# Kernel tuning notes

Measured on AMD Instinct MI355X. Metric: run time of the kernel, lower is better.

Reference implementation:

```python
import jax, jax.numpy as jnp
import numpy as np

B, S, H = 32, 512, 1024
N_CAND = 256
NUM_LABELS = 34


def setup_inputs() -> dict:
    key = jax.random.key(0)
    k1, k2, k3, k4 = jax.random.split(key, 4)
    hidden = jax.random.normal(k1, (B, S, H), dtype=jnp.float32)
    W = jax.random.normal(k2, (2 * H, NUM_LABELS), dtype=jnp.float32) * 0.02
    b = jnp.zeros((NUM_LABELS,), dtype=jnp.float32)
    cand_batch = jax.random.randint(k3, (N_CAND,), 0, B, dtype=jnp.int32)
    # cut positions in [1, S-1] so both left and right segments are non-empty
    cand_cut = jax.random.randint(k4, (N_CAND,), 1, S, dtype=jnp.int32)
    return {"hidden": hidden, "W": W, "b": b,
            "cand_batch": cand_batch, "cand_cut": cand_cut}


def reference(hidden, W, b, cand_batch, cand_cut):
    # hidden: [B, S, H]; cand_batch/cand_cut: [N]
    S_ = hidden.shape[1]
    x = hidden[cand_batch]                      # [N, S, H] per-candidate sequence
    pos = jnp.arange(S_)                        # [S]
    left = (pos[None, :, None] < cand_cut[:, None, None])  # [N, S, 1]
    neg = jnp.finfo(hidden.dtype).min
    pooledL = jnp.max(jnp.where(left, x, neg), axis=1)      # [N, H] max over tokens < cut
    pooledR = jnp.max(jnp.where(left, neg, x), axis=1)      # [N, H] max over tokens >= cut
    pooled = jnp.concatenate([pooledL, pooledR], axis=-1)   # [N, 2H]
    logits = pooled @ W + b                                  # [N, num_labels]
    return logits
```

## Files before the change

kernel.cpp:

```cpp
#include <hip/hip_runtime.h>
#include <cfloat>


constexpr int S_LEN  = 512;
constexpr int HDIM   = 1024;
constexpr int NLAB   = 34;
constexpr int CHUNK  = 16;
constexpr int NCHUNK = S_LEN / CHUNK;

__device__ __forceinline__ void fmax4(float4& a, const float4 v) {
    a.x = fmaxf(a.x, v.x); a.y = fmaxf(a.y, v.y);
    a.z = fmaxf(a.z, v.z); a.w = fmaxf(a.w, v.w);
}

__global__ __launch_bounds__(256) void chunkmax_kernel(
    const float* __restrict__ hidden, float* __restrict__ ws0)
{
    const int blk = blockIdx.x;
    const int b   = blk / NCHUNK;
    const int c   = blk % NCHUNK;
    const int t   = threadIdx.x;

    const float* base = hidden + ((size_t)b * S_LEN + (size_t)c * CHUNK) * HDIM + 4 * t;
    float4 m = make_float4(-FLT_MAX, -FLT_MAX, -FLT_MAX, -FLT_MAX);
    #pragma unroll
    for (int s = 0; s < CHUNK; ++s)
        fmax4(m, *reinterpret_cast<const float4*>(base + (size_t)s * HDIM));

    *reinterpret_cast<float4*>(ws0 + ((size_t)b * NCHUNK + c) * HDIM + 4 * t) = m;
}

__global__ __launch_bounds__(1024) void pool_gemm2(
    const float* __restrict__ hidden,
    const float* __restrict__ ws0,
    const float* __restrict__ W,
    const float* __restrict__ bias,
    const int*   __restrict__ cand_batch,
    const int*   __restrict__ cand_cut,
    float*       __restrict__ out)
{
    __shared__ float partL[4][HDIM];
    __shared__ float partR[4][HDIM];
    __shared__ float pooled[2 * HDIM];
    __shared__ float gpart[16][NLAB];

    const int n   = blockIdx.x;
    const int t   = threadIdx.x;
    const int g   = t >> 8;
    const int tt  = t & 255;
    const int col = 4 * tt;
    const int b   = cand_batch[n];
    const int cut = cand_cut[n];
    const int fcL = cut >> 4;
    const int fcR = (cut + CHUNK - 1) >> 4;

    const float* hbase = hidden + (size_t)b * S_LEN * HDIM + col;
    const float* wbase = ws0 + (size_t)b * NCHUNK * HDIM + col;

    float4 mL = make_float4(-FLT_MAX, -FLT_MAX, -FLT_MAX, -FLT_MAX);
    float4 mR = mL;

    #pragma unroll 2
    for (int c = g; c < fcL; c += 4)
        fmax4(mL, *reinterpret_cast<const float4*>(wbase + (size_t)c * HDIM));
    const int c0 = fcR + ((g - fcR) & 3);
    #pragma unroll 2
    for (int c = c0; c < NCHUNK; c += 4)
        fmax4(mR, *reinterpret_cast<const float4*>(wbase + (size_t)c * HDIM));

    #pragma unroll 2
    for (int s = fcL * CHUNK + g; s < cut; s += 4)
        fmax4(mL, *reinterpret_cast<const float4*>(hbase + (size_t)s * HDIM));
    #pragma unroll 2
    for (int s = cut + g; s < fcR * CHUNK; s += 4)
        fmax4(mR, *reinterpret_cast<const float4*>(hbase + (size_t)s * HDIM));

    *reinterpret_cast<float4*>(&partL[g][col]) = mL;
    *reinterpret_cast<float4*>(&partR[g][col]) = mR;
    __syncthreads();

    {
        const int j = t;
        pooled[j] = fmaxf(fmaxf(partL[0][j], partL[1][j]),
                          fmaxf(partL[2][j], partL[3][j]));
        pooled[HDIM + j] = fmaxf(fmaxf(partR[0][j], partR[1][j]),
                                 fmaxf(partR[2][j], partR[3][j]));
    }
    __syncthreads();

    const int w    = t >> 6;
    const int lane = t & 63;
    if (lane < NLAB) {
        const float* p = pooled + 128 * w;
        const float* Wp = W + (size_t)(128 * w) * NLAB + lane;
        float acc = 0.0f;
        #pragma unroll 8
        for (int k = 0; k < 128; ++k)
            acc = fmaf(p[k], Wp[(size_t)k * NLAB], acc);
        gpart[w][lane] = acc;
    }
    __syncthreads();

    if (t < NLAB) {
        float s = bias[t];
        #pragma unroll
        for (int w2 = 0; w2 < 16; ++w2) s += gpart[w2][t];
        out[(size_t)n * NLAB + t] = s;
    }
}

__global__ __launch_bounds__(256) void dmbert_pool_gemm(
    const float* __restrict__ hidden,
    const float* __restrict__ W,
    const float* __restrict__ bias,
    const int*   __restrict__ cand_batch,
    const int*   __restrict__ cand_cut,
    float*       __restrict__ out)
{
    __shared__ float pooled[2 * HDIM];
    __shared__ float partial[4][NLAB];

    const int n   = blockIdx.x;
    const int t   = threadIdx.x;
    const int bi  = cand_batch[n];
    const int cut = cand_cut[n];

    const float* base = hidden + (size_t)bi * S_LEN * HDIM + 4 * t;
    float4 mL = make_float4(-FLT_MAX, -FLT_MAX, -FLT_MAX, -FLT_MAX);
    float4 mR = mL;

    #pragma unroll 4
    for (int s = 0; s < cut; ++s)
        fmax4(mL, *reinterpret_cast<const float4*>(base + (size_t)s * HDIM));
    #pragma unroll 4
    for (int s = cut; s < S_LEN; ++s)
        fmax4(mR, *reinterpret_cast<const float4*>(base + (size_t)s * HDIM));

    *reinterpret_cast<float4*>(&pooled[4 * t])        = mL;
    *reinterpret_cast<float4*>(&pooled[HDIM + 4 * t]) = mR;
    __syncthreads();

    const int w    = t >> 6;
    const int lane = t & 63;
    if (lane < NLAB) {
        const int k0 = w * (2 * HDIM / 4);
        float acc = 0.0f;
        #pragma unroll 8
        for (int k = k0; k < k0 + (2 * HDIM / 4); ++k)
            acc = fmaf(pooled[k], W[(size_t)k * NLAB + lane], acc);
        partial[w][lane] = acc;
    }
    __syncthreads();

    if (t < NLAB) {
        out[(size_t)n * NLAB + t] =
            partial[0][t] + partial[1][t] + partial[2][t] + partial[3][t] + bias[t];
    }
}

extern "C" void kernel_launch(void* const* d_in, const int* in_sizes, int n_in,
                              void* d_out, int out_size, void* d_ws, size_t ws_size,
                              hipStream_t stream) {
    const float* hidden = (const float*)d_in[0];
    const float* W      = (const float*)d_in[1];
    const float* bias   = (const float*)d_in[2];
    const int*   cb     = (const int*)d_in[3];
    const int*   cc     = (const int*)d_in[4];
    float*       outp   = (float*)d_out;

    const int ncand = in_sizes[3];
    const int B     = in_sizes[0] / (S_LEN * HDIM);
    const size_t ws_needed = (size_t)B * NCHUNK * HDIM * sizeof(float);

    if (ws_size >= ws_needed) {
        float* cm = (float*)d_ws;
        chunkmax_kernel<<<B * NCHUNK, 256, 0, stream>>>(hidden, cm);
        pool_gemm2<<<ncand, 1024, 0, stream>>>(hidden, cm, W, bias, cb, cc, outp);
    } else {
        dmbert_pool_gemm<<<ncand, 256, 0, stream>>>(hidden, W, bias, cb, cc, outp);
    }
}
```

Measured before the change: 107.5 us.

## Precompute prefix/suffix chunk maxima so each candidate reads one row per side

Adds a kernel that builds running prefix and suffix maxima over the per-chunk maxima for each batch. The pooling kernel then takes the full-chunk part of each side from a single precomputed row and scans only the one partial chunk at the cut. This removes the per-candidate loops over up to 32 chunk rows. In exchange it adds a third launch, a serial 32-step scan in a small grid (128 blocks of 128 threads), and extra workspace traffic.

```diff
diff --git a/kernel.cpp b/kernel.cpp
--- a/kernel.cpp
+++ b/kernel.cpp
@@ -7,6 +7,7 @@
 constexpr int NLAB   = 34;
 constexpr int CHUNK  = 16;
 constexpr int NCHUNK = S_LEN / CHUNK;
+constexpr int PSDIM  = NCHUNK + 1;
 
 __device__ __forceinline__ void fmax4(float4& a, const float4 v) {
     a.x = fmaxf(a.x, v.x); a.y = fmaxf(a.y, v.y);
@@ -14,7 +15,7 @@
 }
 
 __global__ __launch_bounds__(256) void chunkmax_kernel(
-    const float* __restrict__ hidden, float* __restrict__ ws0)
+    const float* __restrict__ hidden, float* __restrict__ cm)
 {
     const int blk = blockIdx.x;
     const int b   = blk / NCHUNK;
@@ -27,12 +28,47 @@
     for (int s = 0; s < CHUNK; ++s)
         fmax4(m, *reinterpret_cast<const float4*>(base + (size_t)s * HDIM));
 
-    *reinterpret_cast<float4*>(ws0 + ((size_t)b * NCHUNK + c) * HDIM + 4 * t) = m;
-}
-
-__global__ __launch_bounds__(1024) void pool_gemm2(
+    *reinterpret_cast<float4*>(cm + ((size_t)b * NCHUNK + c) * HDIM + 4 * t) = m;
+}
+
+__global__ __launch_bounds__(128) void prefsuf_kernel(
+    const float* __restrict__ cm,
+    float* __restrict__ pref,
+    float* __restrict__ suff)
+{
+    const int b    = blockIdx.x;
+    const int q    = blockIdx.y;
+    const int tx   = threadIdx.x;
+    const int dir  = tx >> 6;
+    const int lane = tx & 63;
+    const int col  = q * 256 + 4 * lane;
+
+    const float* cmb = cm + (size_t)b * NCHUNK * HDIM + col;
+    float4 run = make_float4(-FLT_MAX, -FLT_MAX, -FLT_MAX, -FLT_MAX);
+
+    if (dir == 0) {
+        float* pb = pref + (size_t)b * PSDIM * HDIM + col;
+        *reinterpret_cast<float4*>(pb) = run;
+        #pragma unroll 8
+        for (int c = 0; c < NCHUNK; ++c) {
+            fmax4(run, *reinterpret_cast<const float4*>(cmb + (size_t)c * HDIM));
+            *reinterpret_cast<float4*>(pb + (size_t)(c + 1) * HDIM) = run;
+        }
+    } else {
+        float* sb = suff + (size_t)b * PSDIM * HDIM + col;
+        *reinterpret_cast<float4*>(sb + (size_t)NCHUNK * HDIM) = run;
+        #pragma unroll 8
+        for (int c = NCHUNK - 1; c >= 0; --c) {
+            fmax4(run, *reinterpret_cast<const float4*>(cmb + (size_t)c * HDIM));
+            *reinterpret_cast<float4*>(sb + (size_t)c * HDIM) = run;
+        }
+    }
+}
+
+__global__ __launch_bounds__(1024) void pool_gemm3(
     const float* __restrict__ hidden,
-    const float* __restrict__ ws0,
+    const float* __restrict__ pref,
+    const float* __restrict__ suff,
     const float* __restrict__ W,
     const float* __restrict__ bias,
     const int*   __restrict__ cand_batch,
@@ -52,46 +88,44 @@
     const int b   = cand_batch[n];
     const int cut = cand_cut[n];
     const int fcL = cut >> 4;
-    const int fcR = (cut + CHUNK - 1) >> 4;
-
-    const float* hbase = hidden + (size_t)b * S_LEN * HDIM + col;
-    const float* wbase = ws0 + (size_t)b * NCHUNK * HDIM + col;
+    const int rem = cut & 15;
+    const int fcR = fcL + (rem ? 1 : 0);
 
     float4 mL = make_float4(-FLT_MAX, -FLT_MAX, -FLT_MAX, -FLT_MAX);
     float4 mR = mL;
 
-    #pragma unroll 2
-    for (int c = g; c < fcL; c += 4)
-        fmax4(mL, *reinterpret_cast<const float4*>(wbase + (size_t)c * HDIM));
-    const int c0 = fcR + ((g - fcR) & 3);
-    #pragma unroll 2
-    for (int c = c0; c < NCHUNK; c += 4)
-        fmax4(mR, *reinterpret_cast<const float4*>(wbase + (size_t)c * HDIM));
-
-    #pragma unroll 2
-    for (int s = fcL * CHUNK + g; s < cut; s += 4)
-        fmax4(mL, *reinterpret_cast<const float4*>(hbase + (size_t)s * HDIM));
-    #pragma unroll 2
-    for (int s = cut + g; s < fcR * CHUNK; s += 4)
-        fmax4(mR, *reinterpret_cast<const float4*>(hbase + (size_t)s * HDIM));
+    if (g == 0)
+        mL = *reinterpret_cast<const float4*>(
+            pref + ((size_t)b * PSDIM + fcL) * HDIM + col);
+    else if (g == 1)
+        mR = *reinterpret_cast<const float4*>(
+            suff + ((size_t)b * PSDIM + fcR) * HDIM + col);
+
+    if (rem) {
+        const int base16 = fcL * CHUNK;
+        const float* hbase = hidden + (size_t)b * S_LEN * HDIM + col;
+        #pragma unroll
+        for (int i = 0; i < 4; ++i) {
+            const int s = base16 + g + 4 * i;
+            const float4 v = *reinterpret_cast<const float4*>(hbase + (size_t)s * HDIM);
+            if (s < cut) fmax4(mL, v); else fmax4(mR, v);
+        }
+    }
 
     *reinterpret_cast<float4*>(&partL[g][col]) = mL;
     *reinterpret_cast<float4*>(&partR[g][col]) = mR;
     __syncthreads();
 
-    {
-        const int j = t;
-        pooled[j] = fmaxf(fmaxf(partL[0][j], partL[1][j]),
-                          fmaxf(partL[2][j], partL[3][j]));
-        pooled[HDIM + j] = fmaxf(fmaxf(partR[0][j], partR[1][j]),
-                                 fmaxf(partR[2][j], partR[3][j]));
-    }
+    pooled[t] = fmaxf(fmaxf(partL[0][t], partL[1][t]),
+                      fmaxf(partL[2][t], partL[3][t]));
+    pooled[HDIM + t] = fmaxf(fmaxf(partR[0][t], partR[1][t]),
+                             fmaxf(partR[2][t], partR[3][t]));
     __syncthreads();
 
     const int w    = t >> 6;
     const int lane = t & 63;
     if (lane < NLAB) {
-        const float* p = pooled + 128 * w;
+        const float* p  = pooled + 128 * w;
         const float* Wp = W + (size_t)(128 * w) * NLAB + lane;
         float acc = 0.0f;
         #pragma unroll 8
@@ -170,12 +204,17 @@
 
     const int ncand = in_sizes[3];
     const int B     = in_sizes[0] / (S_LEN * HDIM);
-    const size_t ws_needed = (size_t)B * NCHUNK * HDIM * sizeof(float);
+    const size_t cm_elems = (size_t)B * NCHUNK * HDIM;
+    const size_t ps_elems = (size_t)B * PSDIM * HDIM;
+    const size_t ws_needed = (cm_elems + 2 * ps_elems) * sizeof(float);
 
     if (ws_size >= ws_needed) {
-        float* cm = (float*)d_ws;
+        float* cm   = (float*)d_ws;
+        float* pref = cm + cm_elems;
+        float* suff = pref + ps_elems;
         chunkmax_kernel<<<B * NCHUNK, 256, 0, stream>>>(hidden, cm);
-        pool_gemm2<<<ncand, 1024, 0, stream>>>(hidden, cm, W, bias, cb, cc, outp);
+        prefsuf_kernel<<<dim3(B, 4), 128, 0, stream>>>(cm, pref, suff);
+        pool_gemm3<<<ncand, 1024, 0, stream>>>(hidden, pref, suff, W, bias, cb, cc, outp);
     } else {
         dmbert_pool_gemm<<<ncand, 256, 0, stream>>>(hidden, W, bias, cb, cc, outp);
     }
```

New measurement: 110.0 us. 2.2% more time.
